# Optimization experiments

Measured on AMD Instinct MI355X. Metric: run time of the kernel, lower is better.

## Reference

```python
import jax, jax.numpy as jnp
import numpy as np

B, N, C, H = 2, 2048, 1024, 16
HD = C // H  # head dim = 64


def setup_inputs() -> dict:
    key = jax.random.key(0)
    kq, kk, kv, km = jax.random.split(key, 4)
    q = jax.random.normal(kq, (B, N, C), dtype=jnp.float32)
    k = jax.random.normal(kk, (B, N, C), dtype=jnp.float32)
    v = jax.random.normal(kv, (B, N, C), dtype=jnp.float32)
    mask = jax.random.randint(km, (B, 1, N, N), 0, 2, dtype=jnp.int32)
    return {"q": q, "k": k, "v": v, "mask": mask}


def reference(q, k, v, mask):
    b, n, c = q.shape
    # (B, N, C) -> (B, H, N, HD)
    qh = q.reshape(b, n, H, HD).transpose(0, 2, 1, 3)
    kh = k.reshape(b, n, H, HD).transpose(0, 2, 1, 3)
    vh = v.reshape(b, n, H, HD).transpose(0, 2, 1, 3)
    scale = 1.0 / jnp.sqrt(jnp.float32(HD))
    # scores: (B, H, N, N)
    scores = jnp.einsum("bhqd,bhkd->bhqk", qh, kh) * scale
    scores = jnp.where(mask == 0, jnp.float32(-1e9), scores)
    probs = jax.nn.softmax(scores, axis=-1)
    atten = jnp.einsum("bhqk,bhkd->bhqd", probs, vh)
    # (B, H, N, HD) -> (B, N, C)
    return atten.transpose(0, 2, 1, 3).reshape(b, n, c)
```

## Files before the change

### kernel.cpp

```cpp
#include <hip/hip_runtime.h>
#include <hip/hip_bf16.h>

#define B_ 2
#define N_ 2048
#define C_ 1024
#define H_ 16
#define HD_ 64

#define KT 64
#define NT (N_ / KT)
#define TILE_E 4096
#define PSTR 72
#define NW 8
#define QB 128

typedef short s16x8 __attribute__((ext_vector_type(8)));
typedef short s16x4 __attribute__((ext_vector_type(4)));
typedef float f32x4 __attribute__((ext_vector_type(4)));

__device__ __forceinline__ ushort f2bf(float x) {
    __hip_bfloat16 h = __float2bfloat16(x);
    return *reinterpret_cast<ushort*>(&h);
}

__device__ __forceinline__ s16x8 cvt8(float4 a, float4 b) {
    union { s16x8 v; __hip_bfloat162 h[4]; } u;
    u.h[0] = __float22bfloat162_rn(float2{a.x, a.y});
    u.h[1] = __float22bfloat162_rn(float2{a.z, a.w});
    u.h[2] = __float22bfloat162_rn(float2{b.x, b.y});
    u.h[3] = __float22bfloat162_rn(float2{b.z, b.w});
    return u.v;
}

__device__ __forceinline__ void gll16(const void* g, void* l) {
    __builtin_amdgcn_global_load_lds(
        (const __attribute__((address_space(1))) unsigned*)g,
        (__attribute__((address_space(3))) unsigned*)l, 16, 0, 0);
}

__global__ __launch_bounds__(256)
void pack_mask(const int* __restrict__ M, unsigned long long* __restrict__ bits) {
    const int gw   = (blockIdx.x * 256 + threadIdx.x) >> 6;
    const int lane = threadIdx.x & 63;
#pragma unroll
    for (int it = 0; it < 16; ++it) {
        const size_t wi = (size_t)gw * 16 + it;
        unsigned long long bal = __ballot(M[wi * 64 + lane] != 0);
        if (lane == 0) bits[wi] = bal;
    }
}

__global__ __launch_bounds__(256)
void conv_k(const float* __restrict__ K, ushort* __restrict__ Kw) {
    const int gt = blockIdx.x * 256 + threadIdx.x;
    const int b  = gt >> 18;
    const int h  = (gt >> 14) & 15;
    const int n  = (gt >> 3) & 2047;
    const int db = gt & 7;
    const size_t src = (size_t)(b * N_ + n) * C_ + h * 64 + db * 8;
    float4 f0 = *(const float4*)(K + src);
    float4 f1 = *(const float4*)(K + src + 4);
    const int key = n & 63, kt = n >> 6;
    ushort* dst = Kw + (size_t)((b * H_ + h) * NT + kt) * TILE_E
                     + key * 64 + ((db ^ (key & 7)) * 8);
    *(s16x8*)dst = cvt8(f0, f1);
}

__global__ __launch_bounds__(256)
void conv_v(const float* __restrict__ V, ushort* __restrict__ Vw) {
    const int gt  = blockIdx.x * 256 + threadIdx.x;
    const int b   = gt >> 16;
    const int h   = (gt >> 12) & 15;
    const int kt  = (gt >> 7) & 31;
    const int kb4 = (gt >> 3) & 15;
    const int db  = gt & 7;
    const int key0 = kb4 * 4;
    float f[4][8];
#pragma unroll
    for (int i = 0; i < 4; ++i) {
        const size_t src = (size_t)(b * N_ + kt * 64 + key0 + i) * C_ + h * 64 + db * 8;
        *(float4*)&f[i][0] = *(const float4*)(V + src);
        *(float4*)&f[i][4] = *(const float4*)(V + src + 4);
    }
    ushort* tb = Vw + (size_t)((b * H_ + h) * NT + kt) * TILE_E;
#pragma unroll
    for (int j = 0; j < 8; ++j) {
        const int d = db * 8 + j;
        union { s16x4 v; __hip_bfloat162 h2[2]; } u;
        u.h2[0] = __float22bfloat162_rn(float2{f[0][j], f[1][j]});
        u.h2[1] = __float22bfloat162_rn(float2{f[2][j], f[3][j]});
        *(s16x4*)(tb + d * 64 + (((key0 >> 3) ^ (d & 7)) * 8) + (key0 & 7)) = u.v;
    }
}

__global__ __launch_bounds__(512, 4)
void mha_fwd(const float* __restrict__ Q, const ushort* __restrict__ Kw,
             const ushort* __restrict__ Vw, const unsigned* __restrict__ bits,
             float* __restrict__ O) {
    __shared__ ushort Kl[2][TILE_E];
    __shared__ ushort Vt[2][TILE_E];
    __shared__ ushort Pl[NW][16 * PSTR];

    const int qt   = blockIdx.x;
    const int h    = blockIdx.y;
    const int b    = blockIdx.z;
    const int tid  = threadIdx.x;
    const int w    = tid >> 6;
    const int lane = tid & 63;
    const int l16  = lane & 15;
    const int quad = lane >> 4;

    const size_t head_off = (size_t)b * N_ * C_ + (size_t)h * HD_;
    const int qb = qt * QB + w * 16;

    const float qs = 0.125f * 1.44269504088896f;
    const size_t qoff = head_off + (size_t)(qb + l16) * C_ + quad * 8;
    float4 q0 = *(const float4*)(Q + qoff);
    float4 q1 = *(const float4*)(Q + qoff + 4);
    float4 q2 = *(const float4*)(Q + qoff + 32);
    float4 q3 = *(const float4*)(Q + qoff + 36);
    q0.x*=qs; q0.y*=qs; q0.z*=qs; q0.w*=qs;
    q1.x*=qs; q1.y*=qs; q1.z*=qs; q1.w*=qs;
    q2.x*=qs; q2.y*=qs; q2.z*=qs; q2.w*=qs;
    q3.x*=qs; q3.y*=qs; q3.z*=qs; q3.w*=qs;
    const s16x8 qa0 = cvt8(q0, q1);
    const s16x8 qa1 = cvt8(q2, q3);

    f32x4 acc[4];
#pragma unroll
    for (int c = 0; c < 4; ++c) acc[c] = f32x4{0.f, 0.f, 0.f, 0.f};
    float2 ls2 = {0.f, 0.f};

    const int fbase  = l16 * 64 + ((quad ^ (l16 & 7)) * 8);
    const int pwbase = l16 * PSTR + quad * 4;
    const int prbase = l16 * PSTR + quad * 8;

    const size_t tilebase = (size_t)((b * H_ + h) * NT) * TILE_E;
    const ushort* Kg = Kw + tilebase + (size_t)tid * 8;
    const ushort* Vg = Vw + tilebase + (size_t)tid * 8;

    const unsigned* mq = bits + ((size_t)b * N_ + qb + l16) * (N_ / 32);

    gll16(Kg, &Kl[0][w * 512]);
    gll16(Vg, &Vt[0][w * 512]);
    const ushort* Kg_pf = Kg + TILE_E;
    const ushort* Vg_pf = Vg + TILE_E;

    for (int kt2 = 0; kt2 < NT; kt2 += 2) {
        const uint4 mw = *(const uint4*)mq;  mq += 4;
        const bool pf1 = (kt2 + 2 < NT);
#pragma unroll
        for (int u = 0; u < 2; ++u) {
            __syncthreads();
            if (u == 0 || pf1) {
                gll16(Kg_pf, &Kl[1 - u][w * 512]);
                gll16(Vg_pf, &Vt[1 - u][w * 512]);
                Kg_pf += TILE_E;  Vg_pf += TILE_E;
            }
            const unsigned w0 = u ? mw.z : mw.x;
            const unsigned w1 = u ? mw.w : mw.y;

            f32x4 s[4];
#pragma unroll
            for (int t = 0; t < 4; ++t) {
                s16x8 kb0 = *(const s16x8*)(&Kl[u][fbase + t * 1024]);
                s16x8 kb1 = *(const s16x8*)(&Kl[u][(fbase ^ 32) + t * 1024]);
                f32x4 z = {0.f, 0.f, 0.f, 0.f};
                z = __builtin_amdgcn_mfma_f32_16x16x32_bf16(kb0, qa0, z, 0, 0, 0);
                z = __builtin_amdgcn_mfma_f32_16x16x32_bf16(kb1, qa1, z, 0, 0, 0);
                s[t] = z;
            }

            const unsigned a0 = w0 >> (quad * 4);
            const unsigned a1 = w1 >> (quad * 4);
#pragma unroll
            for (int t = 0; t < 4; ++t) {
                const unsigned aw = (t < 2) ? a0 : a1;
                const int sh = (t & 1) * 16;
                float p0 = exp2f(((aw >> (sh + 0)) & 1u) ? s[t][0] : -1e9f);
                float p1 = exp2f(((aw >> (sh + 1)) & 1u) ? s[t][1] : -1e9f);
                float p2 = exp2f(((aw >> (sh + 2)) & 1u) ? s[t][2] : -1e9f);
                float p3 = exp2f(((aw >> (sh + 3)) & 1u) ? s[t][3] : -1e9f);
                ls2.x += p0 + p2;
                ls2.y += p1 + p3;
                union { s16x4 v; __hip_bfloat162 h2[2]; } uu;
                uu.h2[0] = __float22bfloat162_rn(float2{p0, p1});
                uu.h2[1] = __float22bfloat162_rn(float2{p2, p3});
                *(s16x4*)(&Pl[w][pwbase + t * 16]) = uu.v;
            }

#pragma unroll
            for (int half = 0; half < 2; ++half) {
                s16x8 pa = *(const s16x8*)(&Pl[w][prbase + half * 32]);
#pragma unroll
                for (int c = 0; c < 4; ++c) {
                    const int vidx = (half ? (fbase ^ 32) : fbase) + c * 1024;
                    s16x8 vb = *(const s16x8*)(&Vt[u][vidx]);
                    acc[c] = __builtin_amdgcn_mfma_f32_16x16x32_bf16(pa, vb, acc[c], 0, 0, 0);
                }
            }
        }
    }

    float lsum = ls2.x + ls2.y;
    lsum += __shfl_xor(lsum, 16);
    lsum += __shfl_xor(lsum, 32);

#pragma unroll
    for (int r = 0; r < 4; ++r) {
        const float inv = 1.0f / __shfl(lsum, quad * 4 + r);
        const size_t obase = head_off + (size_t)(qb + quad * 4 + r) * C_;
        O[obase + l16]      = acc[0][r] * inv;
        O[obase + l16 + 16] = acc[1][r] * inv;
        O[obase + l16 + 32] = acc[2][r] * inv;
        O[obase + l16 + 48] = acc[3][r] * inv;
    }
}

#define KSTR 72
#define VSTR 72
__global__ __launch_bounds__(512, 4)
void mha_fwd_fb(const float* __restrict__ Q, const float* __restrict__ K,
                const float* __restrict__ V, const unsigned* __restrict__ bits,
                float* __restrict__ O) {
    __shared__ ushort Kl[2][KT * KSTR];
    __shared__ ushort Vt[2][HD_ * VSTR];
    __shared__ ushort Pl[NW][16 * PSTR];
    const int qt = blockIdx.x, h = blockIdx.y, b = blockIdx.z, tid = threadIdx.x;
    const int w = tid >> 6, lane = tid & 63, l16 = lane & 15, quad = lane >> 4;
    const size_t head_off = (size_t)b * N_ * C_ + (size_t)h * HD_;
    const int qb = qt * QB + w * 16;
    const float qs = 0.125f * 1.44269504088896f;
    const size_t qoff = head_off + (size_t)(qb + l16) * C_ + quad * 8;
    float4 q0 = *(const float4*)(Q + qoff);
    float4 q1 = *(const float4*)(Q + qoff + 4);
    float4 q2 = *(const float4*)(Q + qoff + 32);
    float4 q3 = *(const float4*)(Q + qoff + 36);
    q0.x*=qs; q0.y*=qs; q0.z*=qs; q0.w*=qs;
    q1.x*=qs; q1.y*=qs; q1.z*=qs; q1.w*=qs;
    q2.x*=qs; q2.y*=qs; q2.z*=qs; q2.w*=qs;
    q3.x*=qs; q3.y*=qs; q3.z*=qs; q3.w*=qs;
    const s16x8 qa0 = cvt8(q0, q1);
    const s16x8 qa1 = cvt8(q2, q3);
    f32x4 acc[4];
#pragma unroll
    for (int c = 0; c < 4; ++c) acc[c] = f32x4{0.f, 0.f, 0.f, 0.f};
    float lsum = 0.f;
    const int skey = tid >> 3, sd0 = (tid & 7) * 8;
    const int kp = tid >> 4, vd0 = (tid & 15) * 4;
    const int vcol = 2 * (kp & 3) + ((((kp >> 2) ^ (vd0 >> 3)) & 7) << 3);
    const unsigned* brow = bits + ((size_t)b * N_ + qb + l16) * (N_ / 32);
    const float SHIFT = 16.0f;
    {
        const size_t kbase = head_off + (size_t)skey * C_ + sd0;
        float4 kA = *(const float4*)(K + kbase);
        float4 kB = *(const float4*)(K + kbase + 4);
        *(s16x8*)(&Kl[0][skey * KSTR + sd0]) = cvt8(kA, kB);
        const size_t vbase = head_off + (size_t)(2 * kp) * C_ + vd0;
        float4 vA = *(const float4*)(V + vbase);
        float4 vB = *(const float4*)(V + vbase + C_);
        const float* ap = (const float*)&vA;
        const float* bp = (const float*)&vB;
#pragma unroll
        for (int i = 0; i < 4; ++i) {
            __hip_bfloat162 pr = __float22bfloat162_rn(float2{ap[i], bp[i]});
            *(unsigned*)(&Vt[0][(vd0 + i) * VSTR + vcol]) = *(unsigned*)&pr;
        }
    }
    for (int kt = 0; kt < NT; ++kt) {
        const int cur = kt & 1;
        float4 kA, kB, vA, vB;
        const bool has_next = (kt + 1 < NT);
        if (has_next) {
            const size_t kbase = head_off + (size_t)((kt + 1) * KT + skey) * C_ + sd0;
            kA = *(const float4*)(K + kbase);
            kB = *(const float4*)(K + kbase + 4);
            const size_t vbase = head_off + (size_t)((kt + 1) * KT + 2 * kp) * C_ + vd0;
            vA = *(const float4*)(V + vbase);
            vB = *(const float4*)(V + vbase + C_);
        }
        const unsigned w0 = brow[2 * kt];
        const unsigned w1 = brow[2 * kt + 1];
        __syncthreads();
        f32x4 s[4];
#pragma unroll
        for (int t = 0; t < 4; ++t) {
            s16x8 kb0 = *(const s16x8*)(&Kl[cur][(t * 16 + l16) * KSTR + quad * 8]);
            s16x8 kb1 = *(const s16x8*)(&Kl[cur][(t * 16 + l16) * KSTR + quad * 8 + 32]);
            f32x4 z = {0.f, 0.f, 0.f, 0.f};
            z = __builtin_amdgcn_mfma_f32_16x16x32_bf16(kb0, qa0, z, 0, 0, 0);
            z = __builtin_amdgcn_mfma_f32_16x16x32_bf16(kb1, qa1, z, 0, 0, 0);
            s[t] = z;
        }
        const unsigned a0 = w0 >> (quad * 4);
        const unsigned a1 = w1 >> (quad * 4);
#pragma unroll
        for (int t = 0; t < 4; ++t) {
            const unsigned aw = (t < 2) ? a0 : a1;
            const int sh = (t & 1) * 16;
            float p0 = exp2f((((aw >> (sh + 0)) & 1u) ? s[t][0] : -1e9f) - SHIFT);
            float p1 = exp2f((((aw >> (sh + 1)) & 1u) ? s[t][1] : -1e9f) - SHIFT);
            float p2 = exp2f((((aw >> (sh + 2)) & 1u) ? s[t][2] : -1e9f) - SHIFT);
            float p3 = exp2f((((aw >> (sh + 3)) & 1u) ? s[t][3] : -1e9f) - SHIFT);
            lsum += (p0 + p1) + (p2 + p3);
            union { s16x4 v; __hip_bfloat162 h2[2]; } uu;
            uu.h2[0] = __float22bfloat162_rn(float2{p0, p1});
            uu.h2[1] = __float22bfloat162_rn(float2{p2, p3});
            *(s16x4*)(&Pl[w][l16 * PSTR + t * 16 + quad * 4]) = uu.v;
        }
#pragma unroll
        for (int half = 0; half < 2; ++half) {
            s16x8 pa = *(const s16x8*)(&Pl[w][l16 * PSTR + half * 32 + quad * 8]);
#pragma unroll
            for (int c = 0; c < 4; ++c) {
                const int dr = c * 16 + l16;
                const int blk = (half * 4 + quad) ^ ((dr >> 3) & 7);
                s16x8 vb = *(const s16x8*)(&Vt[cur][dr * VSTR + blk * 8]);
                acc[c] = __builtin_amdgcn_mfma_f32_16x16x32_bf16(pa, vb, acc[c], 0, 0, 0);
            }
        }
        if (has_next) {
            *(s16x8*)(&Kl[1 - cur][skey * KSTR + sd0]) = cvt8(kA, kB);
            const float* ap = (const float*)&vA;
            const float* bp = (const float*)&vB;
#pragma unroll
            for (int i = 0; i < 4; ++i) {
                __hip_bfloat162 pr = __float22bfloat162_rn(float2{ap[i], bp[i]});
                *(unsigned*)(&Vt[1 - cur][(vd0 + i) * VSTR + vcol]) = *(unsigned*)&pr;
            }
        }
    }
    lsum += __shfl_xor(lsum, 16);
    lsum += __shfl_xor(lsum, 32);
#pragma unroll
    for (int r = 0; r < 4; ++r) {
        const float inv = 1.0f / __shfl(lsum, quad * 4 + r);
        const size_t obase = head_off + (size_t)(qb + quad * 4 + r) * C_;
        O[obase + l16]      = acc[0][r] * inv;
        O[obase + l16 + 16] = acc[1][r] * inv;
        O[obase + l16 + 32] = acc[2][r] * inv;
        O[obase + l16 + 48] = acc[3][r] * inv;
    }
}

extern "C" void kernel_launch(void* const* d_in, const int* in_sizes, int n_in,
                              void* d_out, int out_size, void* d_ws, size_t ws_size,
                              hipStream_t stream) {
    const float* q = (const float*)d_in[0];
    const float* k = (const float*)d_in[1];
    const float* v = (const float*)d_in[2];
    const int*   m = (const int*)d_in[3];
    float*       o = (float*)d_out;

    const size_t BITS_BYTES = (size_t)B_ * N_ * N_ / 8;
    const size_t KV_BYTES   = (size_t)B_ * H_ * N_ * HD_ * 2;
    const size_t NEED       = BITS_BYTES + 2 * KV_BYTES;

    unsigned long long* bits = (unsigned long long*)d_ws;
    hipLaunchKernelGGL(pack_mask, dim3(2048), dim3(256), 0, stream, m, bits);

    dim3 grid(N_ / QB, H_, B_);
    if (ws_size >= NEED) {
        ushort* kw = (ushort*)((char*)d_ws + BITS_BYTES);
        ushort* vw = (ushort*)((char*)d_ws + BITS_BYTES + KV_BYTES);
        hipLaunchKernelGGL(conv_k, dim3(2048), dim3(256), 0, stream, k, kw);
        hipLaunchKernelGGL(conv_v, dim3(512), dim3(256), 0, stream, v, vw);
        hipLaunchKernelGGL(mha_fwd, grid, dim3(512), 0, stream,
                           q, kw, vw, (const unsigned*)bits, o);
    } else {
        hipLaunchKernelGGL(mha_fwd_fb, grid, dim3(512), 0, stream,
                           q, k, v, (const unsigned*)bits, o);
    }
}
```

Baseline: 186.2 us.

## Merge prepass kernels, shrink attention blocks, swizzle P tile, add priorities

Merges the mask-packing, K conversion and V conversion kernels into one prepass launch to cut launch overhead. The attention kernel now uses 256-thread blocks with 64 queries each on a flat 1024-block grid, with a block-index remap that groups heads and batches. It also adds an XOR-swizzled P tile in LDS instead of padding, prefetches the next mask word one iteration ahead, uses the raw exp2 builtin, and raises wave priority around the MFMA sections. Smaller blocks double the K/V tile loads per query and add more synchronization per unit of work.

```diff
diff --git a/kernel.cpp b/kernel.cpp
--- a/kernel.cpp
+++ b/kernel.cpp
@@ -13,6 +13,9 @@
 #define PSTR 72
 #define NW 8
 #define QB 128
+
+#define NWM 4
+#define QBM 64
 
 typedef short s16x8 __attribute__((ext_vector_type(8)));
 typedef short s16x4 __attribute__((ext_vector_type(4)));
@@ -51,59 +54,75 @@
 }
 
 __global__ __launch_bounds__(256)
-void conv_k(const float* __restrict__ K, ushort* __restrict__ Kw) {
-    const int gt = blockIdx.x * 256 + threadIdx.x;
-    const int b  = gt >> 18;
-    const int h  = (gt >> 14) & 15;
-    const int n  = (gt >> 3) & 2047;
-    const int db = gt & 7;
-    const size_t src = (size_t)(b * N_ + n) * C_ + h * 64 + db * 8;
-    float4 f0 = *(const float4*)(K + src);
-    float4 f1 = *(const float4*)(K + src + 4);
-    const int key = n & 63, kt = n >> 6;
-    ushort* dst = Kw + (size_t)((b * H_ + h) * NT + kt) * TILE_E
-                     + key * 64 + ((db ^ (key & 7)) * 8);
-    *(s16x8*)dst = cvt8(f0, f1);
-}
-
-__global__ __launch_bounds__(256)
-void conv_v(const float* __restrict__ V, ushort* __restrict__ Vw) {
-    const int gt  = blockIdx.x * 256 + threadIdx.x;
-    const int b   = gt >> 16;
-    const int h   = (gt >> 12) & 15;
-    const int kt  = (gt >> 7) & 31;
-    const int kb4 = (gt >> 3) & 15;
-    const int db  = gt & 7;
-    const int key0 = kb4 * 4;
-    float f[4][8];
-#pragma unroll
-    for (int i = 0; i < 4; ++i) {
-        const size_t src = (size_t)(b * N_ + kt * 64 + key0 + i) * C_ + h * 64 + db * 8;
-        *(float4*)&f[i][0] = *(const float4*)(V + src);
-        *(float4*)&f[i][4] = *(const float4*)(V + src + 4);
-    }
-    ushort* tb = Vw + (size_t)((b * H_ + h) * NT + kt) * TILE_E;
-#pragma unroll
-    for (int j = 0; j < 8; ++j) {
-        const int d = db * 8 + j;
-        union { s16x4 v; __hip_bfloat162 h2[2]; } u;
-        u.h2[0] = __float22bfloat162_rn(float2{f[0][j], f[1][j]});
-        u.h2[1] = __float22bfloat162_rn(float2{f[2][j], f[3][j]});
-        *(s16x4*)(tb + d * 64 + (((key0 >> 3) ^ (d & 7)) * 8) + (key0 & 7)) = u.v;
-    }
-}
-
-__global__ __launch_bounds__(512, 4)
+void prepass(const int* __restrict__ M, const float* __restrict__ K,
+             const float* __restrict__ V, unsigned long long* __restrict__ bits,
+             ushort* __restrict__ Kw, ushort* __restrict__ Vw) {
+    const int bid = blockIdx.x;
+    const int tid = threadIdx.x;
+    if (bid < 2048) {
+        const int gw   = (bid * 256 + tid) >> 6;
+        const int lane = tid & 63;
+#pragma unroll
+        for (int it = 0; it < 16; ++it) {
+            const size_t wi = (size_t)gw * 16 + it;
+            unsigned long long bal = __ballot(M[wi * 64 + lane] != 0);
+            if (lane == 0) bits[wi] = bal;
+        }
+    } else if (bid < 4096) {
+        const int gt = (bid - 2048) * 256 + tid;
+        const int b  = gt >> 18;
+        const int h  = (gt >> 14) & 15;
+        const int n  = (gt >> 3) & 2047;
+        const int db = gt & 7;
+        const size_t src = (size_t)(b * N_ + n) * C_ + h * 64 + db * 8;
+        float4 f0 = *(const float4*)(K + src);
+        float4 f1 = *(const float4*)(K + src + 4);
+        const int key = n & 63, kt = n >> 6;
+        ushort* dst = Kw + (size_t)((b * H_ + h) * NT + kt) * TILE_E
+                         + key * 64 + ((db ^ (key & 7)) * 8);
+        *(s16x8*)dst = cvt8(f0, f1);
+    } else {
+        const int gt  = (bid - 4096) * 256 + tid;
+        const int b   = gt >> 16;
+        const int h   = (gt >> 12) & 15;
+        const int kt  = (gt >> 7) & 31;
+        const int kb4 = (gt >> 3) & 15;
+        const int db  = gt & 7;
+        const int key0 = kb4 * 4;
+        float f[4][8];
+#pragma unroll
+        for (int i = 0; i < 4; ++i) {
+            const size_t src = (size_t)(b * N_ + kt * 64 + key0 + i) * C_ + h * 64 + db * 8;
+            *(float4*)&f[i][0] = *(const float4*)(V + src);
+            *(float4*)&f[i][4] = *(const float4*)(V + src + 4);
+        }
+        ushort* tb = Vw + (size_t)((b * H_ + h) * NT + kt) * TILE_E;
+#pragma unroll
+        for (int j = 0; j < 8; ++j) {
+            const int d = db * 8 + j;
+            union { s16x4 v; __hip_bfloat162 h2[2]; } u;
+            u.h2[0] = __float22bfloat162_rn(float2{f[0][j], f[1][j]});
+            u.h2[1] = __float22bfloat162_rn(float2{f[2][j], f[3][j]});
+            *(s16x4*)(tb + d * 64 + (((key0 >> 3) ^ (d & 7)) * 8) + (key0 & 7)) = u.v;
+        }
+    }
+}
+
+__global__ __launch_bounds__(256, 4)
 void mha_fwd(const float* __restrict__ Q, const ushort* __restrict__ Kw,
              const ushort* __restrict__ Vw, const unsigned* __restrict__ bits,
              float* __restrict__ O) {
     __shared__ ushort Kl[2][TILE_E];
     __shared__ ushort Vt[2][TILE_E];
-    __shared__ ushort Pl[NW][16 * PSTR];
-
-    const int qt   = blockIdx.x;
-    const int h    = blockIdx.y;
-    const int b    = blockIdx.z;
+    __shared__ ushort Pl[NWM][16 * 64];
+
+    const int sid = blockIdx.x;
+    const int jj  = sid >> 3;
+    const int hb  = ((sid & 7) << 2) | (jj & 3);
+    const int qt  = jj >> 2;
+    const int h   = hb & 15;
+    const int b   = hb >> 4;
+
     const int tid  = threadIdx.x;
     const int w    = tid >> 6;
     const int lane = tid & 63;
@@ -111,7 +130,7 @@
     const int quad = lane >> 4;
 
     const size_t head_off = (size_t)b * N_ * C_ + (size_t)h * HD_;
-    const int qb = qt * QB + w * 16;
+    const int qb = qt * QBM + w * 16;
 
     const float qs = 0.125f * 1.44269504088896f;
     const size_t qoff = head_off + (size_t)(qb + l16) * C_ + quad * 8;
@@ -131,9 +150,9 @@
     for (int c = 0; c < 4; ++c) acc[c] = f32x4{0.f, 0.f, 0.f, 0.f};
     float2 ls2 = {0.f, 0.f};
 
-    const int fbase  = l16 * 64 + ((quad ^ (l16 & 7)) * 8);
-    const int pwbase = l16 * PSTR + quad * 4;
-    const int prbase = l16 * PSTR + quad * 8;
+    const int fbase = l16 * 64 + ((quad ^ (l16 & 7)) * 8);
+    const int prow  = l16 * 64;
+    const int pswz  = (l16 & 7) << 1;
 
     const size_t tilebase = (size_t)((b * H_ + h) * NT) * TILE_E;
     const ushort* Kg = Kw + tilebase + (size_t)tid * 8;
@@ -141,26 +160,33 @@
 
     const unsigned* mq = bits + ((size_t)b * N_ + qb + l16) * (N_ / 32);
 
-    gll16(Kg, &Kl[0][w * 512]);
-    gll16(Vg, &Vt[0][w * 512]);
+    gll16(Kg,        &Kl[0][w * 512]);
+    gll16(Kg + 2048, &Kl[0][w * 512 + 2048]);
+    gll16(Vg,        &Vt[0][w * 512]);
+    gll16(Vg + 2048, &Vt[0][w * 512 + 2048]);
     const ushort* Kg_pf = Kg + TILE_E;
     const ushort* Vg_pf = Vg + TILE_E;
 
+    uint4 mw = *(const uint4*)mq;  mq += 4;
+
     for (int kt2 = 0; kt2 < NT; kt2 += 2) {
-        const uint4 mw = *(const uint4*)mq;  mq += 4;
+        const uint4 mw_nxt = *(const uint4*)mq;  mq += 4;
         const bool pf1 = (kt2 + 2 < NT);
 #pragma unroll
         for (int u = 0; u < 2; ++u) {
             __syncthreads();
             if (u == 0 || pf1) {
-                gll16(Kg_pf, &Kl[1 - u][w * 512]);
-                gll16(Vg_pf, &Vt[1 - u][w * 512]);
+                gll16(Kg_pf,        &Kl[1 - u][w * 512]);
+                gll16(Kg_pf + 2048, &Kl[1 - u][w * 512 + 2048]);
+                gll16(Vg_pf,        &Vt[1 - u][w * 512]);
+                gll16(Vg_pf + 2048, &Vt[1 - u][w * 512 + 2048]);
                 Kg_pf += TILE_E;  Vg_pf += TILE_E;
             }
             const unsigned w0 = u ? mw.z : mw.x;
             const unsigned w1 = u ? mw.w : mw.y;
 
             f32x4 s[4];
+            __builtin_amdgcn_s_setprio(1);
 #pragma unroll
             for (int t = 0; t < 4; ++t) {
                 s16x8 kb0 = *(const s16x8*)(&Kl[u][fbase + t * 1024]);
@@ -170,6 +196,7 @@
                 z = __builtin_amdgcn_mfma_f32_16x16x32_bf16(kb1, qa1, z, 0, 0, 0);
                 s[t] = z;
             }
+            __builtin_amdgcn_s_setprio(0);
 
             const unsigned a0 = w0 >> (quad * 4);
             const unsigned a1 = w1 >> (quad * 4);
@@ -177,21 +204,23 @@
             for (int t = 0; t < 4; ++t) {
                 const unsigned aw = (t < 2) ? a0 : a1;
                 const int sh = (t & 1) * 16;
-                float p0 = exp2f(((aw >> (sh + 0)) & 1u) ? s[t][0] : -1e9f);
-                float p1 = exp2f(((aw >> (sh + 1)) & 1u) ? s[t][1] : -1e9f);
-                float p2 = exp2f(((aw >> (sh + 2)) & 1u) ? s[t][2] : -1e9f);
-                float p3 = exp2f(((aw >> (sh + 3)) & 1u) ? s[t][3] : -1e9f);
+                float p0 = __builtin_amdgcn_exp2f(((aw >> (sh + 0)) & 1u) ? s[t][0] : -1e9f);
+                float p1 = __builtin_amdgcn_exp2f(((aw >> (sh + 1)) & 1u) ? s[t][1] : -1e9f);
+                float p2 = __builtin_amdgcn_exp2f(((aw >> (sh + 2)) & 1u) ? s[t][2] : -1e9f);
+                float p3 = __builtin_amdgcn_exp2f(((aw >> (sh + 3)) & 1u) ? s[t][3] : -1e9f);
                 ls2.x += p0 + p2;
                 ls2.y += p1 + p3;
                 union { s16x4 v; __hip_bfloat162 h2[2]; } uu;
                 uu.h2[0] = __float22bfloat162_rn(float2{p0, p1});
                 uu.h2[1] = __float22bfloat162_rn(float2{p2, p3});
-                *(s16x4*)(&Pl[w][pwbase + t * 16]) = uu.v;
-            }
-
+                *(s16x4*)(&Pl[w][prow + ((((t << 2) | quad) ^ pswz) << 2)]) = uu.v;
+            }
+
+            __builtin_amdgcn_s_setprio(1);
 #pragma unroll
             for (int half = 0; half < 2; ++half) {
-                s16x8 pa = *(const s16x8*)(&Pl[w][prbase + half * 32]);
+                s16x8 pa = *(const s16x8*)(
+                    &Pl[w][prow + ((((half << 3) | (quad << 1)) ^ pswz) << 2)]);
 #pragma unroll
                 for (int c = 0; c < 4; ++c) {
                     const int vidx = (half ? (fbase ^ 32) : fbase) + c * 1024;
@@ -199,7 +228,9 @@
                     acc[c] = __builtin_amdgcn_mfma_f32_16x16x32_bf16(pa, vb, acc[c], 0, 0, 0);
                 }
             }
-        }
+            __builtin_amdgcn_s_setprio(0);
+        }
+        mw = mw_nxt;
     }
 
     float lsum = ls2.x + ls2.y;
@@ -357,17 +388,17 @@
     const size_t NEED       = BITS_BYTES + 2 * KV_BYTES;
 
     unsigned long long* bits = (unsigned long long*)d_ws;
-    hipLaunchKernelGGL(pack_mask, dim3(2048), dim3(256), 0, stream, m, bits);
-
-    dim3 grid(N_ / QB, H_, B_);
+
     if (ws_size >= NEED) {
         ushort* kw = (ushort*)((char*)d_ws + BITS_BYTES);
         ushort* vw = (ushort*)((char*)d_ws + BITS_BYTES + KV_BYTES);
-        hipLaunchKernelGGL(conv_k, dim3(2048), dim3(256), 0, stream, k, kw);
-        hipLaunchKernelGGL(conv_v, dim3(512), dim3(256), 0, stream, v, vw);
-        hipLaunchKernelGGL(mha_fwd, grid, dim3(512), 0, stream,
+        hipLaunchKernelGGL(prepass, dim3(4608), dim3(256), 0, stream,
+                           m, k, v, bits, kw, vw);
+        hipLaunchKernelGGL(mha_fwd, dim3(1024), dim3(256), 0, stream,
                            q, kw, vw, (const unsigned*)bits, o);
     } else {
+        hipLaunchKernelGGL(pack_mask, dim3(2048), dim3(256), 0, stream, m, bits);
+        dim3 grid(N_ / QB, H_, B_);
         hipLaunchKernelGGL(mha_fwd_fb, grid, dim3(512), 0, stream,
                            q, k, v, (const unsigned*)bits, o);
     }
```

Result: faster. 174.1 us (-6.5%).
